# Optimization experiments

Hardware: AMD Instinct MI355X
Metric: run time of the kernel (lower is better)

Reference implementation:

```python
import jax, jax.numpy as jnp
import numpy as np

TEMP1, TEMP2, TEMP3 = 4.0, 5.0, 10.0
NORM_EPS = 1e-12   # F.normalize eps
COS_EPS = 1e-8     # custom_cosine_similarity eps


def setup_inputs() -> dict:
    key = jax.random.key(0)
    k1, k2 = jax.random.split(key)
    vis_embeds = jax.random.normal(k1, (16, 16, 16, 16, 128), dtype=jnp.float32)
    txt_embeds = jax.random.normal(k2, (16, 64, 128), dtype=jnp.float32)
    return {"vis_embeds": vis_embeds, "txt_embeds": txt_embeds}


def reference(vis_embeds, txt_embeds):
    # vis_embeds: [bs, h, w, d, E]; txt_embeds: [bs, T, E] (uniform token_len)
    bs, h, w, d, E = vis_embeds.shape
    S = h * w * d
    # L2-normalize along embedding dim (F.normalize)
    vn = vis_embeds / jnp.clip(jnp.linalg.norm(vis_embeds, axis=-1, keepdims=True), NORM_EPS)
    vn = vn.reshape(bs, S, E)                      # context, flattened source
    tn = txt_embeds / jnp.clip(jnp.linalg.norm(txt_embeds, axis=-1, keepdims=True), NORM_EPS)
    # attention_fn, vectorized over the outer loop index i (txt sample):
    # attn0[i,b,s,t] = <context_b[s], query_i[t]>
    attn0 = jnp.einsum('bse,ite->ibst', vn, tn)    # [bs_txt, bs_vis, S, T]
    s1 = jax.nn.softmax(attn0, axis=-1)            # softmax over query tokens t
    a = jax.nn.softmax(TEMP1 * jnp.swapaxes(s1, -1, -2), axis=-1)  # [i,b,t,s], softmax over s
    # weighted context: [i,b,t,E]
    wc = jnp.einsum('ibts,bse->ibte', a, vn)
    # custom cosine similarity along E between txt tokens and weighted context
    num = jnp.einsum('ibte,ite->ibt', wc, tn)
    w1 = jnp.linalg.norm(tn, axis=-1)              # [i,t] (== 1 up to normalize eps)
    w2 = jnp.linalg.norm(wc, axis=-1)              # [i,b,t]
    cos = num / jnp.clip(w1[:, None, :] * w2, COS_EPS)
    # row_sim: mul temp2, exp, sum over tokens (agg='sum'), log
    row = jnp.log(jnp.sum(jnp.exp(TEMP2 * cos), axis=-1))  # [i_txt, b_vis]
    sims = row.T * TEMP3                           # [b_vis, i_txt] matches torch cat(dim=1)
    labels = jnp.arange(bs)
    logp0 = jax.nn.log_softmax(sims, axis=-1)
    logp1 = jax.nn.log_softmax(sims.T, axis=-1)
    loss0 = -jnp.mean(logp0[labels, labels])
    loss1 = -jnp.mean(logp1[labels, labels])
    loss = (loss0 + loss1) / 2.0
    # att_maps: for sample i the original keeps attn[i] -> diagonal of [i,b,...]
    att_maps = a[labels, labels].reshape(bs, -1, h, w, d)  # [bs, T, h, w, d]
    return loss, att_maps
```

## Files before the change

### kernel.cpp

```cpp
#include <hip/hip_runtime.h>

constexpr int BS = 16;
constexpr int S  = 4096;
constexpr int E  = 128;
constexpr int T  = 64;
constexpr int NSP = 4;
constexpr int SSEG = S / NSP;
constexpr int CH = 128;
constexpr int NCH = SSEG / CH;
constexpr int ETS = 136;
constexpr int TNS = 136;
constexpr int PTS = 264;

constexpr long VN_OFF  = 0;
constexpr long VNT_OFF = (long)BS * S * E;
constexpr long WS_P    = (long)BS * S * E;
constexpr long WS_SIMS = WS_P + (long)256 * NSP * 8192;

typedef __attribute__((ext_vector_type(8))) short bf16x8;
typedef __attribute__((ext_vector_type(4))) float f32x4;

__device__ __forceinline__ unsigned short f2bf(float x) {
    unsigned u = __float_as_uint(x);
    u += 0x7FFFu + ((u >> 16) & 1u);
    return (unsigned short)(u >> 16);
}
__device__ __forceinline__ float bf2f(unsigned short v) {
    return __uint_as_float(((unsigned)v) << 16);
}

__global__ __launch_bounds__(512, 2)
void prep_kernel(const float* __restrict__ vis, unsigned short* __restrict__ wsv)
{
    __shared__ unsigned short Lt[128 * PTS];
    const int tid  = threadIdx.x;
    const int b    = blockIdx.x >> 5;
    const int tile = blockIdx.x & 31;
    const int s0   = tile * 128;
    const float* visb = vis + ((long)b * S + s0) * E;
    unsigned short* vn  = wsv + VN_OFF  + ((long)b * S + s0) * E;
    unsigned short* vnT = wsv + VNT_OFF + (long)b * E * S;

    {
        const int pp = tid >> 3, ee = tid & 7;
        const float* rA = visb + (long)(pp << 1) * E + (ee << 1);
        float2 va[8], vb[8];
        float sa = 0.f, sb = 0.f;
#pragma unroll
        for (int k = 0; k < 8; ++k) {
            va[k] = *(const float2*)(rA + (k << 4));
            vb[k] = *(const float2*)(rA + E + (k << 4));
            sa = fmaf(va[k].x, va[k].x, fmaf(va[k].y, va[k].y, sa));
            sb = fmaf(vb[k].x, vb[k].x, fmaf(vb[k].y, vb[k].y, sb));
        }
        sa += __shfl_xor(sa, 1); sa += __shfl_xor(sa, 2); sa += __shfl_xor(sa, 4);
        sb += __shfl_xor(sb, 1); sb += __shfl_xor(sb, 2); sb += __shfl_xor(sb, 4);
        const float ia = 1.0f / fmaxf(sqrtf(sa), 1e-12f);
        const float ib = 1.0f / fmaxf(sqrtf(sb), 1e-12f);
        const long r0 = (long)(pp << 1) * E, r1 = r0 + E;
#pragma unroll
        for (int k = 0; k < 8; ++k) {
            const int e0 = (ee << 1) + (k << 4);
            const unsigned ax = f2bf(va[k].x * ia), ay = f2bf(va[k].y * ia);
            const unsigned bx = f2bf(vb[k].x * ib), by = f2bf(vb[k].y * ib);
            *(unsigned*)&Lt[e0 * PTS + (pp << 1)]       = ax | (bx << 16);
            *(unsigned*)&Lt[(e0 + 1) * PTS + (pp << 1)] = ay | (by << 16);
            *(unsigned*)&vn[r0 + e0] = ax | (ay << 16);
            *(unsigned*)&vn[r1 + e0] = bx | (by << 16);
        }
    }
    __syncthreads();
    {
        const int e = tid >> 2, sseg = (tid & 3) << 5;
#pragma unroll
        for (int k = 0; k < 4; ++k) {
            const bf16x8 v = *(const bf16x8*)&Lt[e * PTS + sseg + (k << 3)];
            *(bf16x8*)&vnT[(long)e * S + s0 + sseg + (k << 3)] = v;
        }
    }
}

__global__ __launch_bounds__(512, 4)
void clip_main_kernel(const unsigned short* __restrict__ wsv,
                      const float* __restrict__ txt,
                      float* __restrict__ d_out,
                      float* __restrict__ wsf)
{
    __shared__ unsigned short ET[T * ETS];
    __shared__ unsigned short tnL[T * TNS];

    const int tid = threadIdx.x;
    const int w   = tid >> 6;
    const int l   = tid & 63;
    const int cl  = l & 15;
    const int q   = l >> 4;
    const int b   = blockIdx.x & 15;
    const int i   = (blockIdx.x >> 4) & 15;
    const int qt  = blockIdx.x >> 8;
    const bool diag = (i == b);

    const unsigned short* vnb  = wsv + VN_OFF  + (long)b * S * E;
    const unsigned short* vntb = wsv + VNT_OFF + (long)b * E * S;
    float* attb = d_out + 1 + (long)b * (long)T * S;

    const unsigned short* bfp = vnb  + (long)(qt * SSEG + (w << 4) + cl) * E + (q << 3);
    const unsigned short* arp = vntb + (long)((w << 4) + cl) * S + qt * SSEG + (q << 3);

    bf16x8 Bf[4];
#pragma unroll
    for (int kk = 0; kk < 4; ++kk) Bf[kk] = *(const bf16x8*)(bfp + (kk << 5));

    {
        const int r = tid >> 3, seg = tid & 7;
        const float* tp = txt + ((long)i * T + r) * E + (seg << 4);
        const float4 a0 = *(const float4*)(tp);
        const float4 a1 = *(const float4*)(tp + 4);
        const float4 a2 = *(const float4*)(tp + 8);
        const float4 a3 = *(const float4*)(tp + 12);
        float ssq = a0.x*a0.x + a0.y*a0.y + a0.z*a0.z + a0.w*a0.w
                  + a1.x*a1.x + a1.y*a1.y + a1.z*a1.z + a1.w*a1.w
                  + a2.x*a2.x + a2.y*a2.y + a2.z*a2.z + a2.w*a2.w
                  + a3.x*a3.x + a3.y*a3.y + a3.z*a3.z + a3.w*a3.w;
        ssq += __shfl_xor(ssq, 1); ssq += __shfl_xor(ssq, 2); ssq += __shfl_xor(ssq, 4);
        const float inv = 1.0f / fmaxf(sqrtf(ssq), 1e-12f);
        bf16x8 f0, f1;
        f0[0]=(short)f2bf(a0.x*inv); f0[1]=(short)f2bf(a0.y*inv);
        f0[2]=(short)f2bf(a0.z*inv); f0[3]=(short)f2bf(a0.w*inv);
        f0[4]=(short)f2bf(a1.x*inv); f0[5]=(short)f2bf(a1.y*inv);
        f0[6]=(short)f2bf(a1.z*inv); f0[7]=(short)f2bf(a1.w*inv);
        f1[0]=(short)f2bf(a2.x*inv); f1[1]=(short)f2bf(a2.y*inv);
        f1[2]=(short)f2bf(a2.z*inv); f1[3]=(short)f2bf(a2.w*inv);
        f1[4]=(short)f2bf(a3.x*inv); f1[5]=(short)f2bf(a3.y*inv);
        f1[6]=(short)f2bf(a3.z*inv); f1[7]=(short)f2bf(a3.w*inv);
        *(bf16x8*)&tnL[r * TNS + (seg << 4)]     = f0;
        *(bf16x8*)&tnL[r * TNS + (seg << 4) + 8] = f1;
    }
    __syncthreads();

    f32x4 acc2[4];
#pragma unroll
    for (int n = 0; n < 4; ++n) acc2[n] = (f32x4){0.f,0.f,0.f,0.f};

    for (int ch = 0; ch < NCH; ++ch) {
        const int s0 = qt * SSEG + ch * CH;

        bf16x8 aV[4];
        {
            const unsigned short* ar = arp + ch * CH;
#pragma unroll
            for (int kk2 = 0; kk2 < 4; ++kk2) aV[kk2] = *(const bf16x8*)(ar + (kk2 << 5));
        }
        bf16x8 Bn[4];
        {
            const int chn = (ch < NCH - 1) ? (ch + 1) : ch;
            const unsigned short* rn = bfp + (long)chn * CH * E;
#pragma unroll
            for (int kk = 0; kk < 4; ++kk) Bn[kk] = *(const bf16x8*)(rn + (kk << 5));
        }

        {
            f32x4 acc1[4];
#pragma unroll
            for (int mt = 0; mt < 4; ++mt) acc1[mt] = (f32x4){0.f,0.f,0.f,0.f};
#pragma unroll
            for (int kk = 0; kk < 4; ++kk)
#pragma unroll
                for (int mt = 0; mt < 4; ++mt) {
                    const bf16x8 tA = *(const bf16x8*)&tnL[((mt << 4) + cl) * TNS + (kk << 5) + (q << 3)];
                    acc1[mt] = __builtin_amdgcn_mfma_f32_16x16x32_bf16(tA, Bf[kk], acc1[mt], 0, 0, 0);
                }
            float ex[4][4];
            float ssum = 0.f;
#pragma unroll
            for (int mt = 0; mt < 4; ++mt)
#pragma unroll
                for (int r = 0; r < 4; ++r) {
                    const float v = __expf(acc1[mt][r]);
                    ex[mt][r] = v; ssum += v;
                }
            ssum += __shfl_xor(ssum, 16);
            ssum += __shfl_xor(ssum, 32);
            const float csc = 4.0f / ssum;
            const int sloc = (w << 4) + cl;
#pragma unroll
            for (int mt = 0; mt < 4; ++mt)
#pragma unroll
                for (int r = 0; r < 4; ++r)
                    ET[((mt << 4) + (q << 2) + r) * ETS + sloc] = f2bf(__expf(ex[mt][r] * csc));
        }
        __syncthreads();

#pragma unroll
        for (int kk2 = 0; kk2 < 4; ++kk2) {
#pragma unroll
            for (int n = 0; n < 4; ++n) {
                const bf16x8 bE = *(const bf16x8*)&ET[((n << 4) + cl) * ETS + (kk2 << 5) + (q << 3)];
                acc2[n] = __builtin_amdgcn_mfma_f32_16x16x32_bf16(aV[kk2], bE, acc2[n], 0, 0, 0);
            }
        }

        if (diag) {
            const int t = tid >> 3, sg = (tid & 7) << 4;
            float* ap = attb + (long)t * S + s0 + sg;
            const bf16x8 v0 = *(const bf16x8*)&ET[t * ETS + sg];
            const bf16x8 v1 = *(const bf16x8*)&ET[t * ETS + sg + 8];
#pragma unroll
            for (int j = 0; j < 8; ++j) {
                ap[j]     = bf2f((unsigned short)v0[j]);
                ap[8 + j] = bf2f((unsigned short)v1[j]);
            }
        }
        __syncthreads();

#pragma unroll
        for (int kk = 0; kk < 4; ++kk) Bf[kk] = Bn[kk];
    }

    {
        float* pp = wsf + WS_P + ((long)(((i << 4) + b) << 2) + qt) * 8192;
#pragma unroll
        for (int n = 0; n < 4; ++n)
#pragma unroll
            for (int r = 0; r < 4; ++r)
                pp[((w << 4) + (q << 2) + r) * 64 + (n << 4) + cl] = acc2[n][r];
    }
}

__global__ __launch_bounds__(256, 4)
void post_kernel(float* __restrict__ d_out, const float* __restrict__ txt,
                 float* __restrict__ wsf)
{
    const int tid = threadIdx.x;
    if (blockIdx.x >= BS * T) {
        __shared__ float sA[256], sB[256], sC[256];
        const int pair = blockIdx.x - BS * T;
        const int t = tid & 63, w4 = tid >> 6;
        const int i = pair >> 4, b = pair & 15;
        const float* p0 = wsf + WS_P + (long)pair * NSP * 8192;
        const float* tp = txt + ((long)i * T + t) * E + (w4 << 5);

        float ssq = 0.f, num = 0.f, w2 = 0.f;
#pragma unroll 8
        for (int e = 0; e < 32; ++e) {
            const float tv = tp[e];
            const int idx = ((w4 << 5) + e) * 64 + t;
            const float wc = p0[idx] + p0[idx + 8192] + p0[idx + 16384] + p0[idx + 24576];
            ssq = fmaf(tv, tv, ssq);
            num = fmaf(wc, tv, num);
            w2  = fmaf(wc, wc, w2);
        }
        sA[tid] = ssq; sB[tid] = num; sC[tid] = w2;
        __syncthreads();
        if (tid < 64) {
            const float ss = sA[tid] + sA[64 + tid] + sA[128 + tid] + sA[192 + tid];
            const float nm = sB[tid] + sB[64 + tid] + sB[128 + tid] + sB[192 + tid];
            const float ww = sC[tid] + sC[64 + tid] + sC[128 + tid] + sC[192 + tid];
            const float cosv = (nm / fmaxf(sqrtf(ss), 1e-12f)) / fmaxf(sqrtf(ww), 1e-20f);
            float r = __expf(5.0f * cosv);
#pragma unroll
            for (int m = 1; m < 64; m <<= 1) r += __shfl_xor(r, m);
            if (tid == 0) wsf[WS_SIMS + (b << 4) + i] = 10.0f * logf(r);
        }
        return;
    }
    __shared__ float r4[4];
    const int bt = blockIdx.x;
    float* p = d_out + 1 + (long)bt * 4096;
    float v[16];
    float s = 0.f;
#pragma unroll
    for (int k = 0; k < 16; ++k) { v[k] = p[k * 256 + tid]; s += v[k]; }
#pragma unroll
    for (int m = 1; m < 64; m <<= 1) s += __shfl_xor(s, m);
    if ((tid & 63) == 0) r4[tid >> 6] = s;
    __syncthreads();
    const float inv = 1.0f / (r4[0] + r4[1] + r4[2] + r4[3]);
#pragma unroll
    for (int k = 0; k < 16; ++k) p[k * 256 + tid] = v[k] * inv;
}

__global__ __launch_bounds__(256, 1)
void loss_kernel(const float* __restrict__ wsf, float* __restrict__ d_out)
{
    __shared__ float sm[16][17];
    __shared__ float red[16];
    const int tid = threadIdx.x;
    const int bb = tid >> 4, ii = tid & 15;
    const float x = wsf[WS_SIMS + bb * 16 + ii];
    sm[bb][ii] = x;
    float m = x;
#pragma unroll
    for (int msk = 1; msk < 16; msk <<= 1) m = fmaxf(m, __shfl_xor(m, msk));
    float s = __expf(x - m);
#pragma unroll
    for (int msk = 1; msk < 16; msk <<= 1) s += __shfl_xor(s, msk);
    const float lsm0 = x - m - logf(s);
    __syncthreads();
    const float y = sm[ii][bb];
    float m1 = y;
#pragma unroll
    for (int msk = 1; msk < 16; msk <<= 1) m1 = fmaxf(m1, __shfl_xor(m1, msk));
    float s1 = __expf(y - m1);
#pragma unroll
    for (int msk = 1; msk < 16; msk <<= 1) s1 += __shfl_xor(s1, msk);
    const float lsm1 = y - m1 - logf(s1);
    if (bb == ii) red[bb] = lsm0 + lsm1;
    __syncthreads();
    if (tid == 0) {
        float tot = 0.f;
#pragma unroll
        for (int k = 0; k < 16; ++k) tot += red[k];
        d_out[0] = -tot / 32.0f;
    }
}

extern "C" void kernel_launch(void* const* d_in, const int* in_sizes, int n_in,
                              void* d_out, int out_size, void* d_ws, size_t ws_size,
                              hipStream_t stream)
{
    const float* vis = (const float*)d_in[0];
    const float* txt = (const float*)d_in[1];
    float* out = (float*)d_out;
    unsigned short* wsv = (unsigned short*)d_ws;
    float* wsf = (float*)d_ws;

    hipLaunchKernelGGL(prep_kernel, dim3(512), dim3(512), 0, stream, vis, wsv);
    hipLaunchKernelGGL(clip_main_kernel, dim3(BS * BS * NSP), dim3(512), 0, stream,
                       wsv, txt, out, wsf);
    hipLaunchKernelGGL(post_kernel, dim3(BS * T + BS * BS), dim3(256), 0, stream,
                       out, txt, wsf);
    hipLaunchKernelGGL(loss_kernel, dim3(1), dim3(256), 0, stream, wsf, out);
}
```

Before: 195.3 us.

## Process two S-chunks per barrier pair with double ET buffers and exp2

The main loop now handles two 128-wide chunks per iteration. It keeps two LDS buffers for the exponentiated attention tile, so half as many __syncthreads barriers are needed and the trailing barrier is dropped on the last pair. The register prefetch of the next chunk's B fragment is replaced by loading both chunks' fragments at the top of each pair. __expf is replaced with exp2f with the log2(e) factor folded into the scale. This raises LDS use and register pressure and removes the cross-iteration load overlap, which could hurt occupancy or latency hiding.

```diff
diff --git a/kernel.cpp b/kernel.cpp
--- a/kernel.cpp
+++ b/kernel.cpp
@@ -86,7 +86,8 @@
                       float* __restrict__ d_out,
                       float* __restrict__ wsf)
 {
-    __shared__ unsigned short ET[T * ETS];
+    __shared__ unsigned short ETA[T * ETS];
+    __shared__ unsigned short ETB[T * ETS];
     __shared__ unsigned short tnL[T * TNS];
 
     const int tid = threadIdx.x;
@@ -98,17 +99,7 @@
     const int i   = (blockIdx.x >> 4) & 15;
     const int qt  = blockIdx.x >> 8;
     const bool diag = (i == b);
-
-    const unsigned short* vnb  = wsv + VN_OFF  + (long)b * S * E;
-    const unsigned short* vntb = wsv + VNT_OFF + (long)b * E * S;
-    float* attb = d_out + 1 + (long)b * (long)T * S;
-
-    const unsigned short* bfp = vnb  + (long)(qt * SSEG + (w << 4) + cl) * E + (q << 3);
-    const unsigned short* arp = vntb + (long)((w << 4) + cl) * S + qt * SSEG + (q << 3);
-
-    bf16x8 Bf[4];
-#pragma unroll
-    for (int kk = 0; kk < 4; ++kk) Bf[kk] = *(const bf16x8*)(bfp + (kk << 5));
+    const float LOG2E = 1.44269504f;
 
     {
         const int r = tid >> 3, seg = tid & 7;
@@ -141,21 +132,25 @@
 #pragma unroll
     for (int n = 0; n < 4; ++n) acc2[n] = (f32x4){0.f,0.f,0.f,0.f};
 
-    for (int ch = 0; ch < NCH; ++ch) {
-        const int s0 = qt * SSEG + ch * CH;
-
-        bf16x8 aV[4];
+    const unsigned short* vnb  = wsv + VN_OFF  + (long)b * S * E;
+    const unsigned short* vntb = wsv + VNT_OFF + (long)b * E * S;
+    float* attb = d_out + 1 + (long)b * (long)T * S;
+
+    const unsigned short* bfp = vnb  + (long)(qt * SSEG + (w << 4) + cl) * E + (q << 3);
+    const unsigned short* arp = vntb + (long)((w << 4) + cl) * S + qt * SSEG + (q << 3);
+
+    for (int cp = 0; cp < NCH / 2; ++cp) {
+        const int chA = cp << 1, chB = chA + 1;
+        const int s0A = qt * SSEG + chA * CH;
+        const int s0B = s0A + CH;
+
+        bf16x8 BfA[4], BfB[4];
         {
-            const unsigned short* ar = arp + ch * CH;
-#pragma unroll
-            for (int kk2 = 0; kk2 < 4; ++kk2) aV[kk2] = *(const bf16x8*)(ar + (kk2 << 5));
-        }
-        bf16x8 Bn[4];
-        {
-            const int chn = (ch < NCH - 1) ? (ch + 1) : ch;
-            const unsigned short* rn = bfp + (long)chn * CH * E;
-#pragma unroll
-            for (int kk = 0; kk < 4; ++kk) Bn[kk] = *(const bf16x8*)(rn + (kk << 5));
+            const unsigned short* rA = bfp + (long)chA * CH * E;
+            const unsigned short* rB = bfp + (long)chB * CH * E;
+#pragma unroll
+            for (int kk = 0; kk < 4; ++kk) { BfA[kk] = *(const bf16x8*)(rA + (kk << 5));
+                                             BfB[kk] = *(const bf16x8*)(rB + (kk << 5)); }
         }
 
         {
@@ -167,7 +162,7 @@
 #pragma unroll
                 for (int mt = 0; mt < 4; ++mt) {
                     const bf16x8 tA = *(const bf16x8*)&tnL[((mt << 4) + cl) * TNS + (kk << 5) + (q << 3)];
-                    acc1[mt] = __builtin_amdgcn_mfma_f32_16x16x32_bf16(tA, Bf[kk], acc1[mt], 0, 0, 0);
+                    acc1[mt] = __builtin_amdgcn_mfma_f32_16x16x32_bf16(tA, BfA[kk], acc1[mt], 0, 0, 0);
                 }
             float ex[4][4];
             float ssum = 0.f;
@@ -175,45 +170,92 @@
             for (int mt = 0; mt < 4; ++mt)
 #pragma unroll
                 for (int r = 0; r < 4; ++r) {
-                    const float v = __expf(acc1[mt][r]);
+                    const float v = exp2f(acc1[mt][r] * LOG2E);
                     ex[mt][r] = v; ssum += v;
                 }
             ssum += __shfl_xor(ssum, 16);
             ssum += __shfl_xor(ssum, 32);
-            const float csc = 4.0f / ssum;
+            const float csc = 4.0f * LOG2E / ssum;
             const int sloc = (w << 4) + cl;
 #pragma unroll
             for (int mt = 0; mt < 4; ++mt)
 #pragma unroll
                 for (int r = 0; r < 4; ++r)
-                    ET[((mt << 4) + (q << 2) + r) * ETS + sloc] = f2bf(__expf(ex[mt][r] * csc));
+                    ETA[((mt << 4) + (q << 2) + r) * ETS + sloc] = f2bf(exp2f(ex[mt][r] * csc));
+        }
+
+        {
+            f32x4 acc1[4];
+#pragma unroll
+            for (int mt = 0; mt < 4; ++mt) acc1[mt] = (f32x4){0.f,0.f,0.f,0.f};
+#pragma unroll
+            for (int kk = 0; kk < 4; ++kk)
+#pragma unroll
+                for (int mt = 0; mt < 4; ++mt) {
+                    const bf16x8 tA = *(const bf16x8*)&tnL[((mt << 4) + cl) * TNS + (kk << 5) + (q << 3)];
+                    acc1[mt] = __builtin_amdgcn_mfma_f32_16x16x32_bf16(tA, BfB[kk], acc1[mt], 0, 0, 0);
+                }
+            float ex[4][4];
+            float ssum = 0.f;
+#pragma unroll
+            for (int mt = 0; mt < 4; ++mt)
+#pragma unroll
+                for (int r = 0; r < 4; ++r) {
+                    const float v = exp2f(acc1[mt][r] * LOG2E);
+                    ex[mt][r] = v; ssum += v;
+                }
+            ssum += __shfl_xor(ssum, 16);
+            ssum += __shfl_xor(ssum, 32);
+            const float csc = 4.0f * LOG2E / ssum;
+            const int sloc = (w << 4) + cl;
+#pragma unroll
+            for (int mt = 0; mt < 4; ++mt)
+#pragma unroll
+                for (int r = 0; r < 4; ++r)
+                    ETB[((mt << 4) + (q << 2) + r) * ETS + sloc] = f2bf(exp2f(ex[mt][r] * csc));
         }
         __syncthreads();
 
-#pragma unroll
-        for (int kk2 = 0; kk2 < 4; ++kk2) {
-#pragma unroll
-            for (int n = 0; n < 4; ++n) {
-                const bf16x8 bE = *(const bf16x8*)&ET[((n << 4) + cl) * ETS + (kk2 << 5) + (q << 3)];
-                acc2[n] = __builtin_amdgcn_mfma_f32_16x16x32_bf16(aV[kk2], bE, acc2[n], 0, 0, 0);
+        {
+            const unsigned short* arA = arp + chA * CH;
+            const unsigned short* arB = arp + chB * CH;
+#pragma unroll
+            for (int kk2 = 0; kk2 < 4; ++kk2) {
+                const bf16x8 aVA = *(const bf16x8*)(arA + (kk2 << 5));
+#pragma unroll
+                for (int n = 0; n < 4; ++n) {
+                    const bf16x8 bE = *(const bf16x8*)&ETA[((n << 4) + cl) * ETS + (kk2 << 5) + (q << 3)];
+                    acc2[n] = __builtin_amdgcn_mfma_f32_16x16x32_bf16(aVA, bE, acc2[n], 0, 0, 0);
+                }
+            }
+#pragma unroll
+            for (int kk2 = 0; kk2 < 4; ++kk2) {
+                const bf16x8 aVB = *(const bf16x8*)(arB + (kk2 << 5));
+#pragma unroll
+                for (int n = 0; n < 4; ++n) {
+                    const bf16x8 bE = *(const bf16x8*)&ETB[((n << 4) + cl) * ETS + (kk2 << 5) + (q << 3)];
+                    acc2[n] = __builtin_amdgcn_mfma_f32_16x16x32_bf16(aVB, bE, acc2[n], 0, 0, 0);
+                }
             }
         }
 
         if (diag) {
             const int t = tid >> 3, sg = (tid & 7) << 4;
-            float* ap = attb + (long)t * S + s0 + sg;
-            const bf16x8 v0 = *(const bf16x8*)&ET[t * ETS + sg];
-            const bf16x8 v1 = *(const bf16x8*)&ET[t * ETS + sg + 8];
+            float* apA = attb + (long)t * S + s0A + sg;
+            float* apB = attb + (long)t * S + s0B + sg;
+            const bf16x8 a0 = *(const bf16x8*)&ETA[t * ETS + sg];
+            const bf16x8 a1 = *(const bf16x8*)&ETA[t * ETS + sg + 8];
+            const bf16x8 b0 = *(const bf16x8*)&ETB[t * ETS + sg];
+            const bf16x8 b1 = *(const bf16x8*)&ETB[t * ETS + sg + 8];
 #pragma unroll
             for (int j = 0; j < 8; ++j) {
-                ap[j]     = bf2f((unsigned short)v0[j]);
-                ap[8 + j] = bf2f((unsigned short)v1[j]);
+                apA[j]     = bf2f((unsigned short)a0[j]);
+                apA[8 + j] = bf2f((unsigned short)a1[j]);
+                apB[j]     = bf2f((unsigned short)b0[j]);
+                apB[8 + j] = bf2f((unsigned short)b1[j]);
             }
         }
-        __syncthreads();
-
-#pragma unroll
-        for (int kk = 0; kk < 4; ++kk) Bf[kk] = Bn[kk];
+        if (cp < NCH / 2 - 1) __syncthreads();
     }
 
     {
```

New measurement: 202.9 us. 1.04x slower.
